# Performance work log

Measured on AMD Instinct MI355X. Metric: run time of the kernel, lower is better.

## Reference

```python
import math
import jax, jax.numpy as jnp
import numpy as np

IN_DIM = 512
OUT_DIM = 512
K = 3
EPS = 1e-8


def setup_inputs() -> dict:
    key = jax.random.key(0)
    k1, k2, k3 = jax.random.split(key, 3)
    b, h, w = 8, 64, 64
    x = jax.random.normal(k1, (b, IN_DIM, h, w), dtype=jnp.float32)
    style = jax.random.normal(k2, (b, IN_DIM), dtype=jnp.float32)
    weight = jax.random.normal(k3, (OUT_DIM, IN_DIM, K, K), dtype=jnp.float32)
    bias = jnp.zeros((OUT_DIM,), dtype=jnp.float32)
    return {"x": x, "style": style, "weight": weight, "bias": bias}


def _mod_weights(weight, style):
    # EqualizedWeight scaling: c = 1/sqrt(prod(shape[1:]))
    c = 1.0 / math.sqrt(IN_DIM * K * K)
    w = weight * c                                    # [out, in, k, k]
    ws = w[None] * (style[:, None, :, None, None] + 1.0)  # [b, out, in, k, k]
    sigma_inv = jax.lax.rsqrt(jnp.sum(ws * ws, axis=(2, 3, 4), keepdims=True) + EPS)
    return ws * sigma_inv


def reference(x, style, weight, bias):
    ws = _mod_weights(weight, style)                  # [b, out, in, k, k]

    def conv_one(xi, wi):
        # xi: [in, h, w], wi: [out, in, k, k]
        y = jax.lax.conv_general_dilated(
            xi[None], wi, window_strides=(1, 1), padding="SAME",
            dimension_numbers=("NCHW", "OIHW", "NCHW"))
        return y[0]

    out = jax.vmap(conv_one)(x, ws)                   # [b, out, h, w]
    return out + bias[None, :, None, None]
```

## Files before the change

kernel.cpp:

```cpp
#include <hip/hip_runtime.h>

#define CIN 512
#define COUT 512
#define HH 64
#define WW 64
#define BB 8
#define KTOT 4608

#define XPD 66
#define BUFSH (3 * 66 * 64)
#define ROWB (66 * 128)

typedef __attribute__((ext_vector_type(8))) short short8;
typedef __attribute__((ext_vector_type(4))) float f32x4;

__device__ inline unsigned short f2bf(float f) {
    unsigned int u = __float_as_uint(f);
    u += 0x7FFFu + ((u >> 16) & 1u);
    return (unsigned short)(u >> 16);
}

__device__ inline void gll16(const void* g, void* l) {
    __builtin_amdgcn_global_load_lds(
        (const __attribute__((address_space(1))) unsigned int*)g,
        (__attribute__((address_space(3))) unsigned int*)l, 16, 0, 0);
}

__global__ __launch_bounds__(256) void xpose_kernel(const float* __restrict__ x,
                                                    const float* __restrict__ style,
                                                    unsigned short* __restrict__ xtp) {
    __shared__ float tile[32 * 65];
    __shared__ float sst[32];
    const int ic = blockIdx.x;
    const int y  = blockIdx.y;
    const int b  = blockIdx.z;
    const int t  = threadIdx.x;
    const short8 z8 = (short8){0, 0, 0, 0, 0, 0, 0, 0};
    if (t < 32) sst[t] = style[b * CIN + ic * 32 + t] + 1.0f;
    if (t < 8) {
        const int side = t >> 2, u = t & 3;
        *(short8*)(xtp + ((size_t)(b * XPD + y + 1) * XPD + (side ? 65 : 0)) * 512 +
                   ic * 32 + u * 8) = z8;
    }
    if (y == 0 || y == 63) {
        const int prow = (y == 0) ? 0 : 65;
        for (int e = t; e < 264; e += 256) {
            const int col = e >> 2, u = e & 3;
            *(short8*)(xtp + ((size_t)(b * XPD + prow) * XPD + col) * 512 +
                       ic * 32 + u * 8) = z8;
        }
    }
#pragma unroll
    for (int it = 0; it < 2; ++it) {
        const int m  = it * 256 + t;
        const int ii = m >> 4, xq = m & 15;
        const float4 v = ((const float4*)x)[((size_t)(b * CIN + ic * 32 + ii) * HH + y) * 16 + xq];
        float* tp = &tile[ii * 65 + xq * 4];
        tp[0] = v.x; tp[1] = v.y; tp[2] = v.z; tp[3] = v.w;
    }
    __syncthreads();
    const int xx = t >> 2, ii8 = t & 3;
    short8 v8;
#pragma unroll
    for (int k = 0; k < 8; ++k)
        v8[k] = (short)f2bf(tile[(ii8 * 8 + k) * 65 + xx] * sst[ii8 * 8 + k]);
    *(short8*)(xtp + ((size_t)(b * XPD + y + 1) * XPD + (xx + 1)) * 512 + ic * 32 + ii8 * 8) = v8;
}

__global__ __launch_bounds__(256) void wprep_kernel(const float* __restrict__ weight,
                                                    const float* __restrict__ style,
                                                    unsigned short* __restrict__ wpk,
                                                    float* __restrict__ siginv) {
    __shared__ float q[KTOT];
    __shared__ float sred[4][8];
    const int o = blockIdx.x;
    const int t = threadIdx.x;
    const float* wrow = weight + (size_t)o * KTOT;
    const float cst = 1.0f / sqrtf((float)KTOT);
#pragma unroll
    for (int it = 0; it < 18; ++it) {
        int e = it * 256 + t;
        q[e] = wrow[e] * cst;
    }
    __syncthreads();
    float acc[8] = {0.f, 0.f, 0.f, 0.f, 0.f, 0.f, 0.f, 0.f};
#pragma unroll
    for (int ii = 0; ii < 2; ++ii) {
        const int i = t * 2 + ii;
        float wsq = 0.f;
#pragma unroll
        for (int tap = 0; tap < 9; ++tap) {
            float v = q[i * 9 + tap];
            wsq += v * v;
        }
#pragma unroll
        for (int b = 0; b < 8; ++b) {
            float s = style[b * CIN + i] + 1.0f;
            acc[b] += wsq * s * s;
        }
    }
#pragma unroll
    for (int b = 0; b < 8; ++b) {
        float v = acc[b];
#pragma unroll
        for (int off = 32; off > 0; off >>= 1) v += __shfl_down(v, off, 64);
        if ((t & 63) == 0) sred[t >> 6][b] = v;
    }
    __syncthreads();
    if (t < 8) {
        const float S = sred[0][t] + sred[1][t] + sred[2][t] + sred[3][t];
        siginv[t * COUT + o] = rsqrtf(S + 1e-8f);
    }
    const int g = o >> 4, l15 = o & 15;
    for (int m = t; m < 576; m += 256) {
        int c   = m / 36;
        int rem = m - c * 36;
        int tap = rem >> 2;
        int l4  = rem & 3;
        short8 v;
#pragma unroll
        for (int e = 0; e < 8; ++e)
            v[e] = (short)f2bf(q[(c * 32 + l4 * 8 + e) * 9 + tap]);
        *(short8*)(wpk + ((((size_t)c * 9 + tap) * 32 + g) * 64 + l4 * 16 + l15) * 8) = v;
    }
}

__global__ __launch_bounds__(256, 3) void conv_kernel(const unsigned short* __restrict__ wpk,
                                                      const unsigned short* __restrict__ xtp,
                                                      const float* __restrict__ siginv,
                                                      const float* __restrict__ bias,
                                                      float* __restrict__ out) {
    __shared__ __align__(16) unsigned short xs[2 * BUFSH];
    const int bid = blockIdx.x;
    const int k  = bid & 7;
    const int t  = bid >> 3;
    const int ob = k & 1;
    const int b  = (k >> 1) * 2 + (t >> 6);
    const int yb = t & 63;

    const int tid  = threadIdx.x;
    const int lane = tid & 63;
    const int wid_u = __builtin_amdgcn_readfirstlane(tid >> 6);
    const int l15 = lane & 15, l4 = lane >> 4;
    const int og = wid_u;
    const int g0 = ob * 16 + og * 4;

    const int up = lane & 7;
    const unsigned short* srcq[6];
#pragma unroll
    for (int tq = 0; tq < 6; ++tq) {
        const int sl = (wid_u + tq * 4) * 8 + (lane >> 3);
        const int row = sl / 66, col = sl - row * 66;
        srcq[tq] = xtp + ((size_t)(b * XPD + yb + row) * XPD + col) * 512 +
                   (up ^ (col & 7)) * 8;
    }
    const int col6 = 60 + (lane >> 3);
    const unsigned short* src6 =
        xtp + ((size_t)(b * XPD + yb + 2) * XPD + col6) * 512 + (up ^ (col6 & 7)) * 8;

    int vB[3][2];
#pragma unroll
    for (int kx = 0; kx < 3; ++kx)
#pragma unroll
        for (int ks = 0; ks < 2; ++ks)
            vB[kx][ks] = (l15 + kx) * 128 + (((ks * 4 + l4) ^ ((l15 + kx) & 7)) * 16);

    f32x4 acc[4][4];
#pragma unroll
    for (int mi = 0; mi < 4; ++mi)
#pragma unroll
        for (int j = 0; j < 4; ++j) acc[mi][j] = (f32x4){0.f, 0.f, 0.f, 0.f};

    short8 af[3][4];

    const unsigned short* aP = wpk + (size_t)g0 * 512 + lane * 8;

#define STAGE(bufp, icq)                                                                  \
    do {                                                                                  \
        unsigned short* dbase = xs + (bufp) * BUFSH + wid_u * 512;                        \
        _Pragma("unroll") for (int tq = 0; tq < 6; ++tq)                                  \
            gll16(srcq[tq] + (size_t)(icq) * 64, dbase + tq * 2048);                      \
        if (wid_u == 0 && lane < 48)                                                      \
            gll16(src6 + (size_t)(icq) * 64, xs + (bufp) * BUFSH + 12288);                \
    } while (0)

#define PHASE(s, aPic, cbase)                                                             \
    do {                                                                                  \
        const unsigned short* pA = (aPic) + (size_t)((s) + 2) * 16384;                    \
        _Pragma("unroll") for (int mi = 0; mi < 4; ++mi)                                  \
            af[((s) + 2) % 3][mi] = *(const short8*)(pA + mi * 512);                      \
        short8 bfr[4];                                                                    \
        const char* bp = (const char*)xs + (cbase) +                                      \
                         (((s) % 9) / 3) * ROWB + vB[((s) % 9) % 3][(s) / 9];             \
        _Pragma("unroll") for (int j = 0; j < 4; ++j)                                     \
            bfr[j] = *(const short8*)(bp + j * 2048);                                     \
        __builtin_amdgcn_s_setprio(1);                                                    \
        _Pragma("unroll") for (int mi = 0; mi < 4; ++mi)                                  \
            _Pragma("unroll") for (int j = 0; j < 4; ++j)                                 \
                acc[mi][j] = __builtin_amdgcn_mfma_f32_16x16x32_bf16(                     \
                    af[(s) % 3][mi], bfr[j], acc[mi][j], 0, 0, 0);                        \
        __builtin_amdgcn_s_setprio(0);                                                    \
    } while (0)

    af[0][0] = *(const short8*)(aP + 0 * 512);
    af[0][1] = *(const short8*)(aP + 1 * 512);
    af[0][2] = *(const short8*)(aP + 2 * 512);
    af[0][3] = *(const short8*)(aP + 3 * 512);
    {
        const unsigned short* p1 = aP + 16384;
        af[1][0] = *(const short8*)(p1 + 0 * 512);
        af[1][1] = *(const short8*)(p1 + 1 * 512);
        af[1][2] = *(const short8*)(p1 + 2 * 512);
        af[1][3] = *(const short8*)(p1 + 3 * 512);
    }
    STAGE(0, 0);
    __syncthreads();

#pragma unroll 1
    for (int ic = 0; ic < 8; ++ic) {
        if (ic < 7) STAGE((ic + 1) & 1, ic + 1);
        const unsigned short* aPic = aP + (size_t)ic * (18 * 16384);
        const int cbase = (ic & 1) * (BUFSH * 2);
#pragma unroll
        for (int s = 0; s < 18; ++s) {
            PHASE(s, aPic, cbase);
        }
        __syncthreads();
    }

#pragma unroll
    for (int mi = 0; mi < 4; ++mi) {
        const int obase = ob * 256 + og * 64 + mi * 16 + l4 * 4;
#pragma unroll
        for (int rr = 0; rr < 4; ++rr) {
            const int o = obase + rr;
            const float sv = siginv[b * COUT + o];
            const float bv = bias[o];
            float* orow = out + (((size_t)(b * COUT + o) * HH + yb) << 6);
#pragma unroll
            for (int j = 0; j < 4; ++j) {
                orow[j * 16 + l15] = acc[mi][j][rr] * sv + bv;
            }
        }
    }
#undef STAGE
#undef PHASE
}

extern "C" void kernel_launch(void* const* d_in, const int* in_sizes, int n_in,
                              void* d_out, int out_size, void* d_ws, size_t ws_size,
                              hipStream_t stream) {
    const float* x      = (const float*)d_in[0];
    const float* style  = (const float*)d_in[1];
    const float* weight = (const float*)d_in[2];
    const float* bias   = (const float*)d_in[3];
    float* out = (float*)d_out;

    unsigned short* wpk = (unsigned short*)d_ws;
    unsigned short* xtp = wpk + (size_t)2359296;
    float* siginv = (float*)(xtp + (size_t)BB * XPD * XPD * 512);

    xpose_kernel<<<dim3(16, HH, BB), 256, 0, stream>>>(x, style, xtp);
    wprep_kernel<<<COUT, 256, 0, stream>>>(weight, style, wpk, siginv);
    conv_kernel<<<1024, 256, 0, stream>>>(wpk, xtp, siginv, bias, out);
}
```

Baseline: 160.4 us.

## Switch conv MFMA tiles from 16x16x32 to 32x32x16 with repacked weights

Replaces the 4x4 grid of 16x16x32 bf16 MFMAs per phase with a 2x2 grid of 32x32x16 MFMAs, and repacks the modulated weights into 32-row groups to match the new A-fragment layout. B fragments are read from LDS with a new swizzled addressing. The next weight set is now prefetched across the ic boundary, after the B loads are issued. The aim is fewer LDS fragment reads per FLOP and higher MFMA efficiency, at the cost of a new accumulator layout and reworked epilogue indexing that must stay correct.

```diff
diff --git a/kernel.cpp b/kernel.cpp
--- a/kernel.cpp
+++ b/kernel.cpp
@@ -12,7 +12,7 @@
 #define ROWB (66 * 128)
 
 typedef __attribute__((ext_vector_type(8))) short short8;
-typedef __attribute__((ext_vector_type(4))) float f32x4;
+typedef __attribute__((ext_vector_type(16))) float f32x16;
 
 __device__ inline unsigned short f2bf(float f) {
     unsigned int u = __float_as_uint(f);
@@ -111,17 +111,17 @@
         const float S = sred[0][t] + sred[1][t] + sred[2][t] + sred[3][t];
         siginv[t * COUT + o] = rsqrtf(S + 1e-8f);
     }
-    const int g = o >> 4, l15 = o & 15;
+    const int g32 = o >> 5, lr = o & 31;
     for (int m = t; m < 576; m += 256) {
-        int c   = m / 36;
-        int rem = m - c * 36;
-        int tap = rem >> 2;
-        int l4  = rem & 3;
+        const int c16 = m / 18;
+        const int rem = m - c16 * 18;
+        const int tap = rem >> 1;
+        const int hi  = rem & 1;
         short8 v;
 #pragma unroll
         for (int e = 0; e < 8; ++e)
-            v[e] = (short)f2bf(q[(c * 32 + l4 * 8 + e) * 9 + tap]);
-        *(short8*)(wpk + ((((size_t)c * 9 + tap) * 32 + g) * 64 + l4 * 16 + l15) * 8) = v;
+            v[e] = (short)f2bf(q[(c16 * 16 + hi * 8 + e) * 9 + tap]);
+        *(short8*)(wpk + ((((size_t)c16 * 9 + tap) * 16 + g32) * 64 + hi * 32 + lr) * 8) = v;
     }
 }
 
@@ -141,9 +141,9 @@
     const int tid  = threadIdx.x;
     const int lane = tid & 63;
     const int wid_u = __builtin_amdgcn_readfirstlane(tid >> 6);
-    const int l15 = lane & 15, l4 = lane >> 4;
+    const int l31 = lane & 31, hi = lane >> 5;
     const int og = wid_u;
-    const int g0 = ob * 16 + og * 4;
+    const int g0 = ob * 8 + og * 2;
 
     const int up = lane & 7;
     const unsigned short* srcq[6];
@@ -158,18 +158,16 @@
     const unsigned short* src6 =
         xtp + ((size_t)(b * XPD + yb + 2) * XPD + col6) * 512 + (up ^ (col6 & 7)) * 8;
 
-    int vB[3][2];
+    int vB32[3][2];
 #pragma unroll
     for (int kx = 0; kx < 3; ++kx)
 #pragma unroll
-        for (int ks = 0; ks < 2; ++ks)
-            vB[kx][ks] = (l15 + kx) * 128 + (((ks * 4 + l4) ^ ((l15 + kx) & 7)) * 16);
-
-    f32x4 acc[4][4];
-#pragma unroll
-    for (int mi = 0; mi < 4; ++mi)
-#pragma unroll
-        for (int j = 0; j < 4; ++j) acc[mi][j] = (f32x4){0.f, 0.f, 0.f, 0.f};
+        for (int j = 0; j < 2; ++j)
+            vB32[kx][j] = (j * 32 + l31 + kx) * 128 + ((hi ^ ((l31 + kx) & 7)) * 16);
+
+    f32x16 acc00, acc01, acc10, acc11;
+#pragma unroll
+    for (int r = 0; r < 16; ++r) { acc00[r] = 0.f; acc01[r] = 0.f; acc10[r] = 0.f; acc11[r] = 0.f; }
 
     short8 af[3][4];
 
@@ -184,67 +182,74 @@
             gll16(src6 + (size_t)(icq) * 64, xs + (bufp) * BUFSH + 12288);                \
     } while (0)
 
-#define PHASE(s, aPic, cbase)                                                             \
+#define LOAD_SET32(slot, icv, sv)                                                         \
     do {                                                                                  \
-        const unsigned short* pA = (aPic) + (size_t)((s) + 2) * 16384;                    \
-        _Pragma("unroll") for (int mi = 0; mi < 4; ++mi)                                  \
-            af[((s) + 2) % 3][mi] = *(const short8*)(pA + mi * 512);                      \
-        short8 bfr[4];                                                                    \
-        const char* bp = (const char*)xs + (cbase) +                                      \
-                         (((s) % 9) / 3) * ROWB + vB[((s) % 9) % 3][(s) / 9];             \
-        _Pragma("unroll") for (int j = 0; j < 4; ++j)                                     \
-            bfr[j] = *(const short8*)(bp + j * 2048);                                     \
+        const unsigned short* p0 = aP +                                                   \
+            ((size_t)((icv) * 4 + ((sv) / 9) * 2) * 9 + ((sv) % 9)) * 8192;               \
+        af[slot][0] = *(const short8*)(p0);                                               \
+        af[slot][1] = *(const short8*)(p0 + 512);                                         \
+        af[slot][2] = *(const short8*)(p0 + 73728);                                       \
+        af[slot][3] = *(const short8*)(p0 + 73728 + 512);                                 \
+    } while (0)
+
+#define PHASE32(s)                                                                        \
+    do {                                                                                  \
+        const int kx_ = ((s) % 9) % 3, ky_ = ((s) % 9) / 3, kq0_ = ((s) / 9) * 2;         \
+        const char* brow = (const char*)xs + cbase + ky_ * ROWB;                          \
+        short8 b00 = *(const short8*)(brow + (vB32[kx_][0] ^ (kq0_ << 5)));               \
+        short8 b01 = *(const short8*)(brow + (vB32[kx_][1] ^ (kq0_ << 5)));               \
+        short8 b10 = *(const short8*)(brow + (vB32[kx_][0] ^ ((kq0_ + 1) << 5)));         \
+        short8 b11 = *(const short8*)(brow + (vB32[kx_][1] ^ ((kq0_ + 1) << 5)));         \
+        if ((s) < 16) { LOAD_SET32(((s) + 2) % 3, ic, (s) + 2); }                         \
+        else          { LOAD_SET32(((s) + 2) % 3, ic + 1, (s) - 16); }                    \
         __builtin_amdgcn_s_setprio(1);                                                    \
-        _Pragma("unroll") for (int mi = 0; mi < 4; ++mi)                                  \
-            _Pragma("unroll") for (int j = 0; j < 4; ++j)                                 \
-                acc[mi][j] = __builtin_amdgcn_mfma_f32_16x16x32_bf16(                     \
-                    af[(s) % 3][mi], bfr[j], acc[mi][j], 0, 0, 0);                        \
+        acc00 = __builtin_amdgcn_mfma_f32_32x32x16_bf16(af[(s) % 3][0], b00, acc00, 0, 0, 0); \
+        acc10 = __builtin_amdgcn_mfma_f32_32x32x16_bf16(af[(s) % 3][1], b00, acc10, 0, 0, 0); \
+        acc01 = __builtin_amdgcn_mfma_f32_32x32x16_bf16(af[(s) % 3][0], b01, acc01, 0, 0, 0); \
+        acc11 = __builtin_amdgcn_mfma_f32_32x32x16_bf16(af[(s) % 3][1], b01, acc11, 0, 0, 0); \
+        acc00 = __builtin_amdgcn_mfma_f32_32x32x16_bf16(af[(s) % 3][2], b10, acc00, 0, 0, 0); \
+        acc10 = __builtin_amdgcn_mfma_f32_32x32x16_bf16(af[(s) % 3][3], b10, acc10, 0, 0, 0); \
+        acc01 = __builtin_amdgcn_mfma_f32_32x32x16_bf16(af[(s) % 3][2], b11, acc01, 0, 0, 0); \
+        acc11 = __builtin_amdgcn_mfma_f32_32x32x16_bf16(af[(s) % 3][3], b11, acc11, 0, 0, 0); \
         __builtin_amdgcn_s_setprio(0);                                                    \
     } while (0)
 
-    af[0][0] = *(const short8*)(aP + 0 * 512);
-    af[0][1] = *(const short8*)(aP + 1 * 512);
-    af[0][2] = *(const short8*)(aP + 2 * 512);
-    af[0][3] = *(const short8*)(aP + 3 * 512);
-    {
-        const unsigned short* p1 = aP + 16384;
-        af[1][0] = *(const short8*)(p1 + 0 * 512);
-        af[1][1] = *(const short8*)(p1 + 1 * 512);
-        af[1][2] = *(const short8*)(p1 + 2 * 512);
-        af[1][3] = *(const short8*)(p1 + 3 * 512);
-    }
+    LOAD_SET32(0, 0, 0);
+    LOAD_SET32(1, 0, 1);
     STAGE(0, 0);
     __syncthreads();
 
 #pragma unroll 1
     for (int ic = 0; ic < 8; ++ic) {
         if (ic < 7) STAGE((ic + 1) & 1, ic + 1);
-        const unsigned short* aPic = aP + (size_t)ic * (18 * 16384);
         const int cbase = (ic & 1) * (BUFSH * 2);
 #pragma unroll
         for (int s = 0; s < 18; ++s) {
-            PHASE(s, aPic, cbase);
+            PHASE32(s);
         }
         __syncthreads();
     }
 
 #pragma unroll
-    for (int mi = 0; mi < 4; ++mi) {
-        const int obase = ob * 256 + og * 64 + mi * 16 + l4 * 4;
-#pragma unroll
-        for (int rr = 0; rr < 4; ++rr) {
-            const int o = obase + rr;
+    for (int mi = 0; mi < 2; ++mi) {
+#pragma unroll
+        for (int r = 0; r < 16; ++r) {
+            const int o = ob * 256 + og * 64 + mi * 32 + (r & 3) + 8 * (r >> 2) + 4 * hi;
             const float sv = siginv[b * COUT + o];
             const float bv = bias[o];
             float* orow = out + (((size_t)(b * COUT + o) * HH + yb) << 6);
-#pragma unroll
-            for (int j = 0; j < 4; ++j) {
-                orow[j * 16 + l15] = acc[mi][j][rr] * sv + bv;
+            if (mi == 0) {
+                orow[l31]      = acc00[r] * sv + bv;
+                orow[32 + l31] = acc01[r] * sv + bv;
+            } else {
+                orow[l31]      = acc10[r] * sv + bv;
+                orow[32 + l31] = acc11[r] * sv + bv;
             }
         }
     }
 #undef STAGE
-#undef PHASE
+#undef LOAD_SET32
+#undef PHASE32
 }
 
 extern "C" void kernel_launch(void* const* d_in, const int* in_sizes, int n_in,
```

Measured after the change: 188.4 us. 17.5% more time.
